# Kernel optimization log

Measured on AMD Instinct MI355X. Metric: run time of the kernel, lower is better.

## Reference

```python
import jax, jax.numpy as jnp
import numpy as np

B, S, D, H, DK, DV, DFF = 2, 2048, 512, 8, 64, 64, 2048
EPS = 1e-5

def layer_norm(x, g, b):
    mu = jnp.mean(x, axis=-1, keepdims=True)
    var = jnp.mean(jnp.square(x - mu), axis=-1, keepdims=True)
    return (x - mu) * jax.lax.rsqrt(var + EPS) * g + b

def setup_inputs() -> dict:
    key = jax.random.key(0)
    ks = jax.random.split(key, 12)
    s = 0.02
    return {
        "enc_inputs": jax.random.normal(ks[0], (B, S, D), dtype=jnp.float32),
        "attn_mask": jax.random.randint(ks[1], (B, S, S), 0, 2) == 1,
        "Wq": jax.random.normal(ks[2], (D, H * DK), dtype=jnp.float32) * s,
        "bq": jnp.zeros((H * DK,), jnp.float32),
        "Wk": jax.random.normal(ks[3], (D, H * DK), dtype=jnp.float32) * s,
        "bk": jnp.zeros((H * DK,), jnp.float32),
        "Wv": jax.random.normal(ks[4], (D, H * DV), dtype=jnp.float32) * s,
        "bv": jnp.zeros((H * DV,), jnp.float32),
        "Wo": jax.random.normal(ks[5], (H * DV, D), dtype=jnp.float32) * s,
        "bo": jnp.zeros((D,), jnp.float32),
        "ln1_g": jnp.ones((D,), jnp.float32),
        "ln1_b": jnp.zeros((D,), jnp.float32),
        "W1": jax.random.normal(ks[6], (D, DFF), dtype=jnp.float32) * s,
        "b1": jnp.zeros((DFF,), jnp.float32),
        "W2": jax.random.normal(ks[7], (DFF, D), dtype=jnp.float32) * s,
        "b2": jnp.zeros((D,), jnp.float32),
        "ln2_g": jnp.ones((D,), jnp.float32),
        "ln2_b": jnp.zeros((D,), jnp.float32),
    }

def reference(enc_inputs, attn_mask, Wq, bq, Wk, bk, Wv, bv, Wo, bo,
              ln1_g, ln1_b, W1, b1, W2, b2, ln2_g, ln2_b):
    x = enc_inputs
    # projections -> [B, H, S, dk/dv]
    q = (x @ Wq + bq).reshape(B, S, H, DK).transpose(0, 2, 1, 3)
    k = (x @ Wk + bk).reshape(B, S, H, DK).transpose(0, 2, 1, 3)
    v = (x @ Wv + bv).reshape(B, S, H, DV).transpose(0, 2, 1, 3)
    scores = jnp.einsum('bhqd,bhkd->bhqk', q, k) / np.sqrt(DK).astype(np.float32)
    scores = jnp.where(attn_mask[:, None, :, :], jnp.float32(-1e9), scores)
    attn = jax.nn.softmax(scores, axis=-1)  # [B,H,S,S]
    context = jnp.einsum('bhqk,bhkd->bhqd', attn, v)
    context = context.transpose(0, 2, 1, 3).reshape(B, S, H * DV)
    attn_out = layer_norm(context @ Wo + bo + x, ln1_g, ln1_b)
    # position-wise FFN (1x1 convs == per-token linears)
    h = jax.nn.relu(attn_out @ W1 + b1)
    ffn_out = h @ W2 + b2
    out = layer_norm(ffn_out + attn_out, ln2_g, ln2_b)
    return out, attn
```

## Files before the change

### kernel.cpp

```cpp
#include <hip/hip_runtime.h>
#include <hip/hip_bf16.h>

typedef __bf16 bf16;
typedef __bf16 bf16x8 __attribute__((ext_vector_type(8)));
typedef __bf16 bf16x4 __attribute__((ext_vector_type(4)));
typedef float f32x4 __attribute__((ext_vector_type(4)));

#define S_LEN 2048
#define D_MOD 512
#define NHEAD 8
#define DHEAD 64
#define NBATCH 2

#define GLOAD_LDS(g, l) __builtin_amdgcn_global_load_lds( \
    (const __attribute__((address_space(1))) unsigned int*)(g), \
    (__attribute__((address_space(3))) unsigned int*)(l), 16, 0, 0)

__global__ void detect_kernel(const unsigned char* __restrict__ m, int* __restrict__ flags) {
    __shared__ int s4[4];
    int t = threadIdx.x;
    if (t < 4) s4[t] = 0;
    __syncthreads();
    int c3F = 0, c80p0 = 0, cnzo = 0;
    for (int i = t; i < 4096; i += 256) {
        unsigned b = m[i];
        c3F += (b == 0x3F);
        c80p0 += ((b == 0x80) && ((i & 3) == 0));
        cnzo += ((b != 0) && ((i & 3) != 0));
    }
    atomicAdd(&s4[1], c3F);
    atomicAdd(&s4[2], c80p0);
    atomicAdd(&s4[3], cnzo);
    __syncthreads();
    if (t == 0) {
        int mode;
        if (s4[1] > 0)      mode = (s4[2] > 0) ? 2 : 0;
        else if (s4[3] > 0) mode = 1;
        else                mode = 0;
        flags[1] = mode;
    }
}

__global__ void maskconv_kernel(const unsigned char* __restrict__ m,
                                const int* __restrict__ flags,
                                unsigned char* __restrict__ out) {
    long i = ((long)blockIdx.x * 256 + threadIdx.x) * 4;
    int mode = flags[1];
    uchar4 v;
    if (mode == 0) {
        const int* mi = (const int*)m;
        v.x = (unsigned char)(mi[i + 0] != 0);
        v.y = (unsigned char)(mi[i + 1] != 0);
        v.z = (unsigned char)(mi[i + 2] != 0);
        v.w = (unsigned char)(mi[i + 3] != 0);
    } else if (mode == 1) {
        uchar4 r = *(const uchar4*)(m + i);
        v.x = (r.x != 0); v.y = (r.y != 0); v.z = (r.z != 0); v.w = (r.w != 0);
    } else {
        const unsigned short* ms = (const unsigned short*)m;
        v.x = (unsigned char)(ms[i + 0] != 0);
        v.y = (unsigned char)(ms[i + 1] != 0);
        v.z = (unsigned char)(ms[i + 2] != 0);
        v.w = (unsigned char)(ms[i + 3] != 0);
    }
    *(uchar4*)(out + i) = v;
}

__global__ __launch_bounds__(256) void packA(const float* __restrict__ src,
                                             bf16* __restrict__ outh,
                                             bf16* __restrict__ outl) {
    long i = ((long)blockIdx.x * 256 + threadIdx.x) * 4;
    f32x4 v = *(const f32x4*)(src + i);
    bf16x4 h, l;
    #pragma unroll
    for (int j = 0; j < 4; ++j) {
        bf16 hh = (bf16)v[j];
        h[j] = hh;
        l[j] = (bf16)(v[j] - (float)hh);
    }
    *(bf16x4*)(outh + i) = h;
    *(bf16x4*)(outl + i) = l;
}

__global__ __launch_bounds__(256) void packWT(const float* __restrict__ W,
                                              bf16* __restrict__ outh,
                                              bf16* __restrict__ outl,
                                              int K, int N) {
    __shared__ float tile[64][65];
    int n0 = blockIdx.x * 64, k0 = blockIdx.y * 64;
    int t = threadIdx.x, tx = t & 63, ty = t >> 6;
    #pragma unroll
    for (int r = ty; r < 64; r += 4)
        tile[r][tx] = W[(long)(k0 + r) * N + n0 + tx];
    __syncthreads();
    #pragma unroll
    for (int r = ty; r < 64; r += 4) {
        float v = tile[tx][r];
        bf16 h = (bf16)v;
        long idx = (long)(n0 + r) * K + k0 + tx;
        outh[idx] = h;
        outl[idx] = (bf16)(v - (float)h);
    }
}

__global__ void concat_bias(const float* __restrict__ a, const float* __restrict__ b,
                            const float* __restrict__ c, float* __restrict__ o) {
    int t = blockIdx.x * 256 + threadIdx.x;
    o[t] = (t < 512) ? a[t] : (t < 1024 ? b[t - 512] : c[t - 1024]);
}

template<int BM, int BN, int WR, int WC, int EPI>
__global__ __launch_bounds__(256) void mgemm(
    const bf16* __restrict__ Ahi, const bf16* __restrict__ Alo,
    const bf16* __restrict__ Bth, const bf16* __restrict__ Btl,
    const float* __restrict__ bias, const float* __restrict__ res,
    float* __restrict__ outf, bf16* __restrict__ outh, bf16* __restrict__ outl,
    int M, int N, int K)
{
    constexpr int WM = BM / WR, WN = BN / WC;
    constexpr int FI = WM / 16, FJ = WN / 16;
    constexpr int NCH = (2 * BM + 2 * BN) / 16;
    constexpr int NPW = NCH / 4;
    __shared__ bf16 lds[(2 * BM + 2 * BN) * 32];

    int t = threadIdx.x;
    int lane = t & 63, wave = t >> 6;
    int lm = lane & 15, quad = lane >> 4;
    int wr = wave / WC, wc = wave % WC;
    int m0 = blockIdx.y * BM, n0 = blockIdx.x * BN;

    const bf16* gp[NPW];
    #pragma unroll
    for (int ci = 0; ci < NPW; ++ci) {
        int c = wave * NPW + ci;
        const bf16* src; int row0;
        if (c < BM / 16)                  { src = Ahi; row0 = m0 + c * 16; }
        else if (c < 2 * BM / 16)         { src = Alo; row0 = m0 + (c - BM / 16) * 16; }
        else if (c < (2 * BM + BN) / 16)  { src = Bth; row0 = n0 + (c - 2 * BM / 16) * 16; }
        else                              { src = Btl; row0 = n0 + (c - (2 * BM + BN) / 16) * 16; }
        gp[ci] = src + (long)(row0 + (lane >> 2)) * K + (lane & 3) * 8;
    }
    bf16* ldsw = &lds[wave * NPW * 512];

    f32x4 acc[FI][FJ] = {};

    for (int k0 = 0; k0 < K; k0 += 32) {
        __syncthreads();
        #pragma unroll
        for (int ci = 0; ci < NPW; ++ci)
            GLOAD_LDS(gp[ci] + k0, ldsw + ci * 512);
        __syncthreads();

        bf16x8 ah[FI], al[FI];
        #pragma unroll
        for (int i = 0; i < FI; ++i) {
            int row = wr * WM + i * 16 + lm;
            ah[i] = *(const bf16x8*)&lds[row * 32 + quad * 8];
            al[i] = *(const bf16x8*)&lds[(BM + row) * 32 + quad * 8];
        }
        #pragma unroll
        for (int j = 0; j < FJ; ++j) {
            int row = wc * WN + j * 16 + lm;
            bf16x8 bh = *(const bf16x8*)&lds[(2 * BM + row) * 32 + quad * 8];
            bf16x8 bl = *(const bf16x8*)&lds[(2 * BM + BN + row) * 32 + quad * 8];
            #pragma unroll
            for (int i = 0; i < FI; ++i) {
                acc[i][j] = __builtin_amdgcn_mfma_f32_16x16x32_bf16(ah[i], bh, acc[i][j], 0, 0, 0);
                acc[i][j] = __builtin_amdgcn_mfma_f32_16x16x32_bf16(ah[i], bl, acc[i][j], 0, 0, 0);
                acc[i][j] = __builtin_amdgcn_mfma_f32_16x16x32_bf16(al[i], bh, acc[i][j], 0, 0, 0);
            }
        }
    }

    #pragma unroll
    for (int j = 0; j < FJ; ++j) {
        int gn = n0 + wc * WN + j * 16 + lm;
        float bv = bias[gn];
        #pragma unroll
        for (int i = 0; i < FI; ++i) {
            #pragma unroll
            for (int r = 0; r < 4; ++r) {
                int gm = m0 + wr * WM + i * 16 + quad * 4 + r;
                float v = acc[i][j][r] + bv;
                if (EPI == 3) {
                    if (gn < 512)       outh[(long)gm * 512 + gn] = (bf16)v;
                    else if (gn < 1024) outl[(long)gm * 512 + gn - 512] = (bf16)v;
                    else                outf[(long)gm * 512 + gn - 1024] = v;
                } else {
                    long idx = (long)gm * N + gn;
                    if (EPI == 1) {
                        v = fmaxf(v, 0.f);
                        bf16 h = (bf16)v;
                        outh[idx] = h;
                        outl[idx] = (bf16)(v - (float)h);
                    } else {
                        if (EPI == 2) v += res[idx];
                        outf[idx] = v;
                    }
                }
            }
        }
    }
}

__global__ __launch_bounds__(256) void pack_vT(const float* __restrict__ src,
                                               bf16* __restrict__ dst) {
    __shared__ float tile[64][65];
    int s0 = blockIdx.x * 64;
    int bh = blockIdx.y;
    int b = bh >> 3, h = bh & 7;
    int t = threadIdx.x, tx = t & 63, ty = t >> 6;
    #pragma unroll
    for (int r = ty; r < 64; r += 4)
        tile[r][tx] = src[(long)(b * S_LEN + s0 + r) * 512 + h * 64 + tx];
    __syncthreads();
    #pragma unroll
    for (int d = ty; d < 64; d += 4)
        dst[((long)bh * 64 + d) * S_LEN + s0 + tx] = (bf16)tile[tx][d];
}

__global__ __launch_bounds__(256) void attn_kernel(
    const bf16* __restrict__ Q, const bf16* __restrict__ Kg,
    const bf16* __restrict__ Vt, const unsigned char* __restrict__ mask8,
    float* __restrict__ attnO, bf16* __restrict__ ctxh, bf16* __restrict__ ctxl)
{
    __shared__ bf16 Qs[64][72];
    __shared__ bf16 Ks[64][72];
    __shared__ bf16 Vs[64][72];
    __shared__ bf16 Ps[64][72];

    int t = threadIdx.x;
    int qt = blockIdx.x & 31, bh = blockIdx.x >> 5;
    int b_ = bh >> 3, h_ = bh & 7;
    int q0 = qt * 64;
    int lane = t & 63, wave = t >> 6;
    int lm = lane & 15, quad = lane >> 4, q8 = quad * 8;
    int sr = t >> 2, sc = (t & 3) * 16;

    const bf16* Qp = Q + (((long)(b_ * S_LEN + q0 + sr)) << 9) + (h_ << 6) + sc;
    *(bf16x8*)&Qs[sr][sc]     = *(const bf16x8*)(Qp);
    *(bf16x8*)&Qs[sr][sc + 8] = *(const bf16x8*)(Qp + 8);
    __syncthreads();
    bf16x8 a0 = *(const bf16x8*)&Qs[wave * 16 + lm][q8];
    bf16x8 a1 = *(const bf16x8*)&Qs[wave * 16 + lm][32 + q8];

    float mrow[4], lrow[4];
    #pragma unroll
    for (int r = 0; r < 4; ++r) { mrow[r] = -1e30f; lrow[r] = 0.f; }

    const unsigned char* Mbase = mask8 + (long)b_ * S_LEN * S_LEN;

    for (int kt = 0; kt < 32; ++kt) {
        int k0 = kt * 64;
        __syncthreads();
        const bf16* Kp = Kg + (((long)(b_ * S_LEN + k0 + sr)) << 9) + (h_ << 6) + sc;
        *(bf16x8*)&Ks[sr][sc]     = *(const bf16x8*)(Kp);
        *(bf16x8*)&Ks[sr][sc + 8] = *(const bf16x8*)(Kp + 8);
        __syncthreads();

        f32x4 sacc[4] = {};
        #pragma unroll
        for (int tn = 0; tn < 4; ++tn) {
            bf16x8 b0 = *(const bf16x8*)&Ks[tn * 16 + lm][q8];
            bf16x8 b1 = *(const bf16x8*)&Ks[tn * 16 + lm][32 + q8];
            sacc[tn] = __builtin_amdgcn_mfma_f32_16x16x32_bf16(a0, b0, sacc[tn], 0, 0, 0);
            sacc[tn] = __builtin_amdgcn_mfma_f32_16x16x32_bf16(a1, b1, sacc[tn], 0, 0, 0);
        }
        #pragma unroll
        for (int r = 0; r < 4; ++r) {
            int grow = q0 + wave * 16 + quad * 4 + r;
            const unsigned char* Mr = Mbase + (long)grow * S_LEN + k0 + lm;
            float sv[4];
            float tmax = -1e30f;
            #pragma unroll
            for (int tn = 0; tn < 4; ++tn) {
                float s = sacc[tn][r] * 0.125f;
                if (Mr[tn * 16]) s = -1e9f;
                sv[tn] = s;
                tmax = fmaxf(tmax, s);
            }
            #pragma unroll
            for (int off = 8; off; off >>= 1) tmax = fmaxf(tmax, __shfl_xor(tmax, off));
            float mnew = fmaxf(mrow[r], tmax);
            float es = 0.f;
            #pragma unroll
            for (int tn = 0; tn < 4; ++tn) es += __expf(sv[tn] - mnew);
            #pragma unroll
            for (int off = 8; off; off >>= 1) es += __shfl_xor(es, off);
            lrow[r] = lrow[r] * __expf(mrow[r] - mnew) + es;
            mrow[r] = mnew;
        }
    }
    float rl[4];
    #pragma unroll
    for (int r = 0; r < 4; ++r) rl[r] = 1.f / lrow[r];

    float* attnBase = attnO + (long)bh * S_LEN * S_LEN;
    const bf16* Vbase = Vt + (long)bh * (DHEAD * S_LEN);
    f32x4 oacc[4] = {};

    for (int kt = 0; kt < 32; ++kt) {
        int k0 = kt * 64;
        __syncthreads();
        const bf16* Kp = Kg + (((long)(b_ * S_LEN + k0 + sr)) << 9) + (h_ << 6) + sc;
        *(bf16x8*)&Ks[sr][sc]     = *(const bf16x8*)(Kp);
        *(bf16x8*)&Ks[sr][sc + 8] = *(const bf16x8*)(Kp + 8);
        const bf16* Vp = Vbase + (long)sr * S_LEN + k0 + sc;
        *(bf16x8*)&Vs[sr][sc]     = *(const bf16x8*)(Vp);
        *(bf16x8*)&Vs[sr][sc + 8] = *(const bf16x8*)(Vp + 8);
        __syncthreads();

        f32x4 sacc[4] = {};
        #pragma unroll
        for (int tn = 0; tn < 4; ++tn) {
            bf16x8 b0 = *(const bf16x8*)&Ks[tn * 16 + lm][q8];
            bf16x8 b1 = *(const bf16x8*)&Ks[tn * 16 + lm][32 + q8];
            sacc[tn] = __builtin_amdgcn_mfma_f32_16x16x32_bf16(a0, b0, sacc[tn], 0, 0, 0);
            sacc[tn] = __builtin_amdgcn_mfma_f32_16x16x32_bf16(a1, b1, sacc[tn], 0, 0, 0);
        }
        #pragma unroll
        for (int r = 0; r < 4; ++r) {
            int grow = q0 + wave * 16 + quad * 4 + r;
            const unsigned char* Mr = Mbase + (long)grow * S_LEN + k0 + lm;
            #pragma unroll
            for (int tn = 0; tn < 4; ++tn) {
                float s = sacc[tn][r] * 0.125f;
                if (Mr[tn * 16]) s = -1e9f;
                float p = __expf(s - mrow[r]) * rl[r];
                attnBase[(long)grow * S_LEN + k0 + tn * 16 + lm] = p;
                Ps[wave * 16 + quad * 4 + r][tn * 16 + lm] = (bf16)p;
            }
        }
        __syncthreads();
        bf16x8 pa0 = *(const bf16x8*)&Ps[wave * 16 + lm][q8];
        bf16x8 pa1 = *(const bf16x8*)&Ps[wave * 16 + lm][32 + q8];
        #pragma unroll
        for (int td = 0; td < 4; ++td) {
            bf16x8 v0 = *(const bf16x8*)&Vs[td * 16 + lm][q8];
            bf16x8 v1 = *(const bf16x8*)&Vs[td * 16 + lm][32 + q8];
            oacc[td] = __builtin_amdgcn_mfma_f32_16x16x32_bf16(pa0, v0, oacc[td], 0, 0, 0);
            oacc[td] = __builtin_amdgcn_mfma_f32_16x16x32_bf16(pa1, v1, oacc[td], 0, 0, 0);
        }
    }

    #pragma unroll
    for (int td = 0; td < 4; ++td)
    #pragma unroll
    for (int r = 0; r < 4; ++r) {
        int grow = q0 + wave * 16 + quad * 4 + r;
        long cidx = (((long)(b_ * S_LEN + grow)) << 9) + (h_ << 6) + td * 16 + lm;
        float v = oacc[td][r];
        bf16 h = (bf16)v;
        ctxh[cidx] = h;
        ctxl[cidx] = (bf16)(v - (float)h);
    }
}

template<int SPLIT>
__global__ __launch_bounds__(256) void ln_kernel(
    const float* __restrict__ X, const float* __restrict__ g,
    const float* __restrict__ bb, float* __restrict__ out,
    bf16* __restrict__ oh, bf16* __restrict__ ol)
{
    __shared__ float red[8];
    int row = blockIdx.x, t = threadIdx.x;
    float x0 = X[(long)row * 512 + t];
    float x1 = X[(long)row * 512 + 256 + t];
    float s = x0 + x1, ss = x0 * x0 + x1 * x1;
    #pragma unroll
    for (int off = 32; off; off >>= 1) { s += __shfl_xor(s, off); ss += __shfl_xor(ss, off); }
    if ((t & 63) == 0) { red[t >> 6] = s; red[4 + (t >> 6)] = ss; }
    __syncthreads();
    float S_ = red[0] + red[1] + red[2] + red[3];
    float SS = red[4] + red[5] + red[6] + red[7];
    float mu = S_ * (1.f / 512.f);
    float var = SS * (1.f / 512.f) - mu * mu;
    float is = rsqrtf(var + 1e-5f);
    float o0 = (x0 - mu) * is * g[t]       + bb[t];
    float o1 = (x1 - mu) * is * g[t + 256] + bb[t + 256];
    out[(long)row * 512 + t]       = o0;
    out[(long)row * 512 + 256 + t] = o1;
    if (SPLIT) {
        bf16 h0 = (bf16)o0, h1 = (bf16)o1;
        oh[(long)row * 512 + t]       = h0;
        oh[(long)row * 512 + 256 + t] = h1;
        ol[(long)row * 512 + t]       = (bf16)(o0 - (float)h0);
        ol[(long)row * 512 + 256 + t] = (bf16)(o1 - (float)h1);
    }
}

extern "C" void kernel_launch(void* const* d_in, const int* in_sizes, int n_in,
                              void* d_out, int out_size, void* d_ws, size_t ws_size,
                              hipStream_t stream)
{
    const float* x = (const float*)d_in[0];
    const unsigned char* maskraw = (const unsigned char*)d_in[1];
    const float* Wq = (const float*)d_in[2];  const float* bq = (const float*)d_in[3];
    const float* Wk = (const float*)d_in[4];  const float* bk = (const float*)d_in[5];
    const float* Wv = (const float*)d_in[6];  const float* bv = (const float*)d_in[7];
    const float* Wo = (const float*)d_in[8];  const float* bo = (const float*)d_in[9];
    const float* ln1g = (const float*)d_in[10]; const float* ln1b = (const float*)d_in[11];
    const float* W1 = (const float*)d_in[12]; const float* b1f = (const float*)d_in[13];
    const float* W2 = (const float*)d_in[14]; const float* b2f = (const float*)d_in[15];
    const float* ln2g = (const float*)d_in[16]; const float* ln2b = (const float*)d_in[17];

    float* outMain = (float*)d_out;
    float* outAttn = outMain + (size_t)NBATCH * S_LEN * D_MOD;

    char* w = (char*)d_ws;
    size_t off = 0;
    auto alloc = [&](size_t bytes) -> char* {
        char* p = w + off;
        off += (bytes + 255) & ~(size_t)255;
        return p;
    };
    const size_t MB = 1024 * 1024;
    int* flags = (int*)alloc(256);
    unsigned char* mask8 = (unsigned char*)alloc(8 * MB);

    bf16* xh   = (bf16*)alloc(4 * MB);
    bf16* xl   = (bf16*)alloc(4 * MB);
    bf16* Qb   = (bf16*)alloc(4 * MB);
    bf16* Kb   = (bf16*)alloc(4 * MB);
    float* vf  = (float*)alloc(8 * MB);
    bf16* Vtb  = (bf16*)alloc(4 * MB);
    bf16* ctxh = (bf16*)alloc(4 * MB);
    bf16* ctxl = (bf16*)alloc(4 * MB);
    bf16* hh = xh;
    bf16* hl = (bf16*)vf;

    float* tmp   = (float*)alloc(8 * MB);
    float* aoutf = (float*)alloc(8 * MB);
    bf16* aouth  = (bf16*)alloc(4 * MB);
    bf16* aoutl  = (bf16*)alloc(4 * MB);

    bf16* WqkvTh = (bf16*)alloc((size_t)1536 * 512 * 2);
    bf16* WqkvTl = (bf16*)alloc((size_t)1536 * 512 * 2);
    bf16* WoTh = (bf16*)alloc(512 * 1024); bf16* WoTl = (bf16*)alloc(512 * 1024);
    bf16* W1Th = (bf16*)alloc(2 * MB);     bf16* W1Tl = (bf16*)alloc(2 * MB);
    bf16* W2Th = (bf16*)alloc(2 * MB);     bf16* W2Tl = (bf16*)alloc(2 * MB);
    float* bqkv = (float*)alloc(1536 * 4);

    const int M = NBATCH * S_LEN;

    detect_kernel<<<1, 256, 0, stream>>>(maskraw, flags);
    maskconv_kernel<<<(NBATCH * S_LEN * S_LEN) / 1024, 256, 0, stream>>>(maskraw, flags, mask8);

    concat_bias<<<6, 256, 0, stream>>>(bq, bk, bv, bqkv);
    packWT<<<dim3(8, 8), 256, 0, stream>>>(Wq, WqkvTh,              WqkvTl,              512, 512);
    packWT<<<dim3(8, 8), 256, 0, stream>>>(Wk, WqkvTh + 512 * 512,  WqkvTl + 512 * 512,  512, 512);
    packWT<<<dim3(8, 8), 256, 0, stream>>>(Wv, WqkvTh + 1024 * 512, WqkvTl + 1024 * 512, 512, 512);
    packWT<<<dim3(8, 8), 256, 0, stream>>>(Wo, WoTh, WoTl, 512, 512);
    packWT<<<dim3(32, 8), 256, 0, stream>>>(W1, W1Th, W1Tl, 512, 2048);
    packWT<<<dim3(8, 32), 256, 0, stream>>>(W2, W2Th, W2Tl, 2048, 512);

    packA<<<(M * 512) / 1024, 256, 0, stream>>>(x, xh, xl);
    mgemm<64, 128, 1, 4, 3><<<dim3(12, 64), 256, 0, stream>>>(
        xh, xl, WqkvTh, WqkvTl, bqkv, nullptr, vf, Qb, Kb, M, 1536, 512);
    pack_vT<<<dim3(32, 16), 256, 0, stream>>>(vf, Vtb);

    attn_kernel<<<512, 256, 0, stream>>>(Qb, Kb, Vtb, mask8, outAttn, ctxh, ctxl);

    mgemm<64, 64, 2, 2, 2><<<dim3(8, 64), 256, 0, stream>>>(
        ctxh, ctxl, WoTh, WoTl, bo, x, tmp, nullptr, nullptr, M, 512, 512);
    ln_kernel<1><<<M, 256, 0, stream>>>(tmp, ln1g, ln1b, aoutf, aouth, aoutl);

    mgemm<128, 128, 2, 2, 1><<<dim3(16, 32), 256, 0, stream>>>(
        aouth, aoutl, W1Th, W1Tl, b1f, nullptr, nullptr, hh, hl, M, 2048, 512);
    mgemm<64, 64, 2, 2, 2><<<dim3(8, 64), 256, 0, stream>>>(
        hh, hl, W2Th, W2Tl, b2f, aoutf, tmp, nullptr, nullptr, M, 512, 2048);
    ln_kernel<0><<<M, 256, 0, stream>>>(tmp, ln2g, ln2b, outMain, nullptr, nullptr);

    (void)in_sizes; (void)n_in; (void)out_size; (void)ws_size;
}
```

Before: 656.5 us.

## Replace two-pass attention with online softmax and in-place attn normalization

The attention kernel drops the separate max/sum pass over K and computes the softmax online in a single loop. Raw masked scores are written to the attn output, the context accumulator is rescaled as the max changes, and at the end each block rereads its attn rows to apply exp and normalization in place. This removes a full QK^T recompute and the second K/mask sweep, at the cost of an extra read-modify-write of the large fp32 attn matrix. It also fuses the three QKV weight-pack launches into one.

```diff
diff --git a/kernel.cpp b/kernel.cpp
--- a/kernel.cpp
+++ b/kernel.cpp
@@ -103,6 +103,30 @@
     }
 }
 
+__global__ __launch_bounds__(256) void packWT3(const float* __restrict__ Wa,
+                                               const float* __restrict__ Wb,
+                                               const float* __restrict__ Wc,
+                                               bf16* __restrict__ outh,
+                                               bf16* __restrict__ outl) {
+    __shared__ float tile[64][65];
+    const float* W = blockIdx.z == 0 ? Wa : (blockIdx.z == 1 ? Wb : Wc);
+    long dofs = (long)blockIdx.z * 512 * 512;
+    int n0 = blockIdx.x * 64, k0 = blockIdx.y * 64;
+    int t = threadIdx.x, tx = t & 63, ty = t >> 6;
+    #pragma unroll
+    for (int r = ty; r < 64; r += 4)
+        tile[r][tx] = W[(long)(k0 + r) * 512 + n0 + tx];
+    __syncthreads();
+    #pragma unroll
+    for (int r = ty; r < 64; r += 4) {
+        float v = tile[tx][r];
+        bf16 h = (bf16)v;
+        long idx = dofs + (long)(n0 + r) * 512 + k0 + tx;
+        outh[idx] = h;
+        outl[idx] = (bf16)(v - (float)h);
+    }
+}
+
 __global__ void concat_bias(const float* __restrict__ a, const float* __restrict__ b,
                             const float* __restrict__ c, float* __restrict__ o) {
     int t = blockIdx.x * 256 + threadIdx.x;
@@ -228,6 +252,8 @@
     __shared__ bf16 Ks[64][72];
     __shared__ bf16 Vs[64][72];
     __shared__ bf16 Ps[64][72];
+    __shared__ float mlds[64];
+    __shared__ float llds[64];
 
     int t = threadIdx.x;
     int qt = blockIdx.x & 31, bh = blockIdx.x >> 5;
@@ -247,57 +273,11 @@
     float mrow[4], lrow[4];
     #pragma unroll
     for (int r = 0; r < 4; ++r) { mrow[r] = -1e30f; lrow[r] = 0.f; }
+    f32x4 oacc[4] = {};
 
     const unsigned char* Mbase = mask8 + (long)b_ * S_LEN * S_LEN;
-
-    for (int kt = 0; kt < 32; ++kt) {
-        int k0 = kt * 64;
-        __syncthreads();
-        const bf16* Kp = Kg + (((long)(b_ * S_LEN + k0 + sr)) << 9) + (h_ << 6) + sc;
-        *(bf16x8*)&Ks[sr][sc]     = *(const bf16x8*)(Kp);
-        *(bf16x8*)&Ks[sr][sc + 8] = *(const bf16x8*)(Kp + 8);
-        __syncthreads();
-
-        f32x4 sacc[4] = {};
-        #pragma unroll
-        for (int tn = 0; tn < 4; ++tn) {
-            bf16x8 b0 = *(const bf16x8*)&Ks[tn * 16 + lm][q8];
-            bf16x8 b1 = *(const bf16x8*)&Ks[tn * 16 + lm][32 + q8];
-            sacc[tn] = __builtin_amdgcn_mfma_f32_16x16x32_bf16(a0, b0, sacc[tn], 0, 0, 0);
-            sacc[tn] = __builtin_amdgcn_mfma_f32_16x16x32_bf16(a1, b1, sacc[tn], 0, 0, 0);
-        }
-        #pragma unroll
-        for (int r = 0; r < 4; ++r) {
-            int grow = q0 + wave * 16 + quad * 4 + r;
-            const unsigned char* Mr = Mbase + (long)grow * S_LEN + k0 + lm;
-            float sv[4];
-            float tmax = -1e30f;
-            #pragma unroll
-            for (int tn = 0; tn < 4; ++tn) {
-                float s = sacc[tn][r] * 0.125f;
-                if (Mr[tn * 16]) s = -1e9f;
-                sv[tn] = s;
-                tmax = fmaxf(tmax, s);
-            }
-            #pragma unroll
-            for (int off = 8; off; off >>= 1) tmax = fmaxf(tmax, __shfl_xor(tmax, off));
-            float mnew = fmaxf(mrow[r], tmax);
-            float es = 0.f;
-            #pragma unroll
-            for (int tn = 0; tn < 4; ++tn) es += __expf(sv[tn] - mnew);
-            #pragma unroll
-            for (int off = 8; off; off >>= 1) es += __shfl_xor(es, off);
-            lrow[r] = lrow[r] * __expf(mrow[r] - mnew) + es;
-            mrow[r] = mnew;
-        }
-    }
-    float rl[4];
-    #pragma unroll
-    for (int r = 0; r < 4; ++r) rl[r] = 1.f / lrow[r];
-
     float* attnBase = attnO + (long)bh * S_LEN * S_LEN;
     const bf16* Vbase = Vt + (long)bh * (DHEAD * S_LEN);
-    f32x4 oacc[4] = {};
 
     for (int kt = 0; kt < 32; ++kt) {
         int k0 = kt * 64;
@@ -318,19 +298,44 @@
             sacc[tn] = __builtin_amdgcn_mfma_f32_16x16x32_bf16(a0, b0, sacc[tn], 0, 0, 0);
             sacc[tn] = __builtin_amdgcn_mfma_f32_16x16x32_bf16(a1, b1, sacc[tn], 0, 0, 0);
         }
+
+        float scr[4];
         #pragma unroll
         for (int r = 0; r < 4; ++r) {
             int grow = q0 + wave * 16 + quad * 4 + r;
             const unsigned char* Mr = Mbase + (long)grow * S_LEN + k0 + lm;
+            float sv[4];
+            float tmax = -1e30f;
             #pragma unroll
             for (int tn = 0; tn < 4; ++tn) {
                 float s = sacc[tn][r] * 0.125f;
                 if (Mr[tn * 16]) s = -1e9f;
-                float p = __expf(s - mrow[r]) * rl[r];
-                attnBase[(long)grow * S_LEN + k0 + tn * 16 + lm] = p;
-                Ps[wave * 16 + quad * 4 + r][tn * 16 + lm] = (bf16)p;
+                sv[tn] = s;
+                tmax = fmaxf(tmax, s);
+                attnBase[(long)grow * S_LEN + k0 + tn * 16 + lm] = s;
             }
-        }
+            #pragma unroll
+            for (int off = 8; off; off >>= 1) tmax = fmaxf(tmax, __shfl_xor(tmax, off));
+            float mnew = fmaxf(mrow[r], tmax);
+            float sc0 = __expf(mrow[r] - mnew);
+            float es = 0.f;
+            #pragma unroll
+            for (int tn = 0; tn < 4; ++tn) {
+                float pe = __expf(sv[tn] - mnew);
+                es += pe;
+                Ps[wave * 16 + quad * 4 + r][tn * 16 + lm] = (bf16)pe;
+            }
+            #pragma unroll
+            for (int off = 8; off; off >>= 1) es += __shfl_xor(es, off);
+            lrow[r] = lrow[r] * sc0 + es;
+            mrow[r] = mnew;
+            scr[r] = sc0;
+        }
+        #pragma unroll
+        for (int td = 0; td < 4; ++td)
+            #pragma unroll
+            for (int r = 0; r < 4; ++r) oacc[td][r] *= scr[r];
+
         __syncthreads();
         bf16x8 pa0 = *(const bf16x8*)&Ps[wave * 16 + lm][q8];
         bf16x8 pa1 = *(const bf16x8*)&Ps[wave * 16 + lm][32 + q8];
@@ -343,16 +348,42 @@
         }
     }
 
+    float rl[4];
+    #pragma unroll
+    for (int r = 0; r < 4; ++r) rl[r] = 1.f / lrow[r];
+
     #pragma unroll
     for (int td = 0; td < 4; ++td)
     #pragma unroll
     for (int r = 0; r < 4; ++r) {
         int grow = q0 + wave * 16 + quad * 4 + r;
         long cidx = (((long)(b_ * S_LEN + grow)) << 9) + (h_ << 6) + td * 16 + lm;
-        float v = oacc[td][r];
+        float v = oacc[td][r] * rl[r];
         bf16 h = (bf16)v;
         ctxh[cidx] = h;
         ctxl[cidx] = (bf16)(v - (float)h);
+    }
+
+    if (lm == 0) {
+        #pragma unroll
+        for (int r = 0; r < 4; ++r) {
+            int row = wave * 16 + quad * 4 + r;
+            mlds[row] = mrow[r];
+            llds[row] = rl[r];
+        }
+    }
+    __syncthreads();
+    int rr = t >> 2;
+    float m_ = mlds[rr], rl_ = llds[rr];
+    f32x4* base = (f32x4*)(attnBase + (((long)(q0 + rr)) << 11) + (t & 3) * 512);
+    #pragma unroll 4
+    for (int i = 0; i < 128; ++i) {
+        f32x4 v = base[i];
+        v[0] = __expf(v[0] - m_) * rl_;
+        v[1] = __expf(v[1] - m_) * rl_;
+        v[2] = __expf(v[2] - m_) * rl_;
+        v[3] = __expf(v[3] - m_) * rl_;
+        base[i] = v;
     }
 }
 
@@ -447,9 +478,7 @@
     maskconv_kernel<<<(NBATCH * S_LEN * S_LEN) / 1024, 256, 0, stream>>>(maskraw, flags, mask8);
 
     concat_bias<<<6, 256, 0, stream>>>(bq, bk, bv, bqkv);
-    packWT<<<dim3(8, 8), 256, 0, stream>>>(Wq, WqkvTh,              WqkvTl,              512, 512);
-    packWT<<<dim3(8, 8), 256, 0, stream>>>(Wk, WqkvTh + 512 * 512,  WqkvTl + 512 * 512,  512, 512);
-    packWT<<<dim3(8, 8), 256, 0, stream>>>(Wv, WqkvTh + 1024 * 512, WqkvTl + 1024 * 512, 512, 512);
+    packWT3<<<dim3(8, 8, 3), 256, 0, stream>>>(Wq, Wk, Wv, WqkvTh, WqkvTl);
     packWT<<<dim3(8, 8), 256, 0, stream>>>(Wo, WoTh, WoTl, 512, 512);
     packWT<<<dim3(32, 8), 256, 0, stream>>>(W1, W1Th, W1Tl, 512, 2048);
     packWT<<<dim3(8, 32), 256, 0, stream>>>(W2, W2Th, W2Tl, 2048, 512);
```

After: 789.1 us. 20.2% more time.

## Double-buffer K/V tiles via async global-to-LDS loads and merge weight packing kernels

Applied to the files above, without the earlier changes.

The attention kernel now prefetches the next K and V tiles straight into swizzled, double-buffered LDS with global_load_lds, so loads overlap the current tile's MFMA and softmax work and two barriers per iteration become one. The XOR swizzle replaces the padded layout to avoid LDS bank conflicts. Six weight-transpose launches and the bias concat are merged into one kernel to cut launch overhead. The cost is more LDS per block, which may lower occupancy, and subtle ordering around the Ps buffer and the async-load completion.

```diff
diff --git a/kernel.cpp b/kernel.cpp
--- a/kernel.cpp
+++ b/kernel.cpp
@@ -82,13 +82,36 @@
     *(bf16x4*)(outl + i) = l;
 }
 
-__global__ __launch_bounds__(256) void packWT(const float* __restrict__ W,
-                                              bf16* __restrict__ outh,
-                                              bf16* __restrict__ outl,
-                                              int K, int N) {
+__global__ __launch_bounds__(256) void packW_all(
+    const float* __restrict__ Wq, const float* __restrict__ Wk,
+    const float* __restrict__ Wv, const float* __restrict__ Wo,
+    const float* __restrict__ W1, const float* __restrict__ W2,
+    const float* __restrict__ bq, const float* __restrict__ bk,
+    const float* __restrict__ bv,
+    bf16* __restrict__ WqkvTh, bf16* __restrict__ WqkvTl,
+    bf16* __restrict__ WoTh, bf16* __restrict__ WoTl,
+    bf16* __restrict__ W1Th, bf16* __restrict__ W1Tl,
+    bf16* __restrict__ W2Th, bf16* __restrict__ W2Tl,
+    float* __restrict__ bqkv)
+{
     __shared__ float tile[64][65];
-    int n0 = blockIdx.x * 64, k0 = blockIdx.y * 64;
-    int t = threadIdx.x, tx = t & 63, ty = t >> 6;
+    int blk = blockIdx.x, t = threadIdx.x;
+    if (blk >= 768) {
+        int i = (blk - 768) * 256 + t;
+        bqkv[i] = (i < 512) ? bq[i] : (i < 1024 ? bk[i - 512] : bv[i - 1024]);
+        return;
+    }
+    const float* W; bf16* oh; bf16* ol; int K, N, lb, sh; long dofs = 0;
+    if (blk < 256) {
+        lb = blk & 63; K = 512; N = 512; sh = 3;
+        if (blk < 64)       { W = Wq; oh = WqkvTh; ol = WqkvTl; }
+        else if (blk < 128) { W = Wk; oh = WqkvTh; ol = WqkvTl; dofs = 512 * 512; }
+        else if (blk < 192) { W = Wv; oh = WqkvTh; ol = WqkvTl; dofs = (long)2 * 512 * 512; }
+        else                { W = Wo; oh = WoTh;   ol = WoTl; }
+    } else if (blk < 512) { lb = blk - 256; W = W1; oh = W1Th; ol = W1Tl; K = 512;  N = 2048; sh = 5; }
+    else                  { lb = blk - 512; W = W2; oh = W2Th; ol = W2Tl; K = 2048; N = 512;  sh = 3; }
+    int n0 = (lb & ((1 << sh) - 1)) * 64, k0 = (lb >> sh) * 64;
+    int tx = t & 63, ty = t >> 6;
     #pragma unroll
     for (int r = ty; r < 64; r += 4)
         tile[r][tx] = W[(long)(k0 + r) * N + n0 + tx];
@@ -97,16 +120,10 @@
     for (int r = ty; r < 64; r += 4) {
         float v = tile[tx][r];
         bf16 h = (bf16)v;
-        long idx = (long)(n0 + r) * K + k0 + tx;
-        outh[idx] = h;
-        outl[idx] = (bf16)(v - (float)h);
-    }
-}
-
-__global__ void concat_bias(const float* __restrict__ a, const float* __restrict__ b,
-                            const float* __restrict__ c, float* __restrict__ o) {
-    int t = blockIdx.x * 256 + threadIdx.x;
-    o[t] = (t < 512) ? a[t] : (t < 1024 ? b[t - 512] : c[t - 1024]);
+        long idx = dofs + (long)(n0 + r) * K + k0 + tx;
+        oh[idx] = h;
+        ol[idx] = (bf16)(v - (float)h);
+    }
 }
 
 template<int BM, int BN, int WR, int WC, int EPI>
@@ -225,8 +242,8 @@
     float* __restrict__ attnO, bf16* __restrict__ ctxh, bf16* __restrict__ ctxl)
 {
     __shared__ bf16 Qs[64][72];
-    __shared__ bf16 Ks[64][72];
-    __shared__ bf16 Vs[64][72];
+    __shared__ bf16 Ks[2][64 * 64];
+    __shared__ bf16 Vs[2][64 * 64];
     __shared__ bf16 Ps[64][72];
 
     int t = threadIdx.x;
@@ -237,6 +254,9 @@
     int lm = lane & 15, quad = lane >> 4, q8 = quad * 8;
     int sr = t >> 2, sc = (t & 3) * 16;
 
+    int srow8 = lane >> 3;
+    int sslot = (lane & 7) ^ srow8;
+
     const bf16* Qp = Q + (((long)(b_ * S_LEN + q0 + sr)) << 9) + (h_ << 6) + sc;
     *(bf16x8*)&Qs[sr][sc]     = *(const bf16x8*)(Qp);
     *(bf16x8*)&Qs[sr][sc + 8] = *(const bf16x8*)(Qp + 8);
@@ -249,97 +269,129 @@
     for (int r = 0; r < 4; ++r) { mrow[r] = -1e30f; lrow[r] = 0.f; }
 
     const unsigned char* Mbase = mask8 + (long)b_ * S_LEN * S_LEN;
-
-    for (int kt = 0; kt < 32; ++kt) {
-        int k0 = kt * 64;
+    const bf16* Kbase = Kg + (((long)(b_ * S_LEN)) << 9) + (h_ << 6);
+    const bf16* Vbase = Vt + (long)bh * (DHEAD * S_LEN);
+
+    {
+        #pragma unroll
+        for (int c = 0; c < 2; ++c) {
+            int rl = wave * 16 + c * 8;
+            GLOAD_LDS(Kbase + (long)(rl + srow8) * 512 + sslot * 8, &Ks[0][rl * 64]);
+        }
         __syncthreads();
-        const bf16* Kp = Kg + (((long)(b_ * S_LEN + k0 + sr)) << 9) + (h_ << 6) + sc;
-        *(bf16x8*)&Ks[sr][sc]     = *(const bf16x8*)(Kp);
-        *(bf16x8*)&Ks[sr][sc + 8] = *(const bf16x8*)(Kp + 8);
+        int cur = 0;
+        for (int kt = 0; kt < 32; ++kt) {
+            int k0 = kt * 64;
+            if (kt < 31) {
+                #pragma unroll
+                for (int c = 0; c < 2; ++c) {
+                    int rl = wave * 16 + c * 8;
+                    GLOAD_LDS(Kbase + (long)(k0 + 64 + rl + srow8) * 512 + sslot * 8,
+                              &Ks[cur ^ 1][rl * 64]);
+                }
+            }
+            const bf16* kc = Ks[cur];
+            f32x4 sacc[4] = {};
+            #pragma unroll
+            for (int tn = 0; tn < 4; ++tn) {
+                int row = tn * 16 + lm, sw = row & 7;
+                bf16x8 b0 = *(const bf16x8*)&kc[row * 64 + ((quad ^ sw) << 3)];
+                bf16x8 b1 = *(const bf16x8*)&kc[row * 64 + (((4 | quad) ^ sw) << 3)];
+                sacc[tn] = __builtin_amdgcn_mfma_f32_16x16x32_bf16(a0, b0, sacc[tn], 0, 0, 0);
+                sacc[tn] = __builtin_amdgcn_mfma_f32_16x16x32_bf16(a1, b1, sacc[tn], 0, 0, 0);
+            }
+            #pragma unroll
+            for (int r = 0; r < 4; ++r) {
+                int grow = q0 + wave * 16 + quad * 4 + r;
+                const unsigned char* Mr = Mbase + (long)grow * S_LEN + k0 + lm;
+                float sv[4];
+                float tmax = -1e30f;
+                #pragma unroll
+                for (int tn = 0; tn < 4; ++tn) {
+                    float s = sacc[tn][r] * 0.125f;
+                    if (Mr[tn * 16]) s = -1e9f;
+                    sv[tn] = s;
+                    tmax = fmaxf(tmax, s);
+                }
+                #pragma unroll
+                for (int off = 8; off; off >>= 1) tmax = fmaxf(tmax, __shfl_xor(tmax, off));
+                float mnew = fmaxf(mrow[r], tmax);
+                float es = 0.f;
+                #pragma unroll
+                for (int tn = 0; tn < 4; ++tn) es += __expf(sv[tn] - mnew);
+                #pragma unroll
+                for (int off = 8; off; off >>= 1) es += __shfl_xor(es, off);
+                lrow[r] = lrow[r] * __expf(mrow[r] - mnew) + es;
+                mrow[r] = mnew;
+            }
+            __syncthreads();
+            cur ^= 1;
+        }
+    }
+    float rl4[4];
+    #pragma unroll
+    for (int r = 0; r < 4; ++r) rl4[r] = 1.f / lrow[r];
+
+    float* attnBase = attnO + (long)bh * S_LEN * S_LEN;
+    f32x4 oacc[4] = {};
+
+    {
+        #pragma unroll
+        for (int c = 0; c < 2; ++c) {
+            int rl = wave * 16 + c * 8;
+            GLOAD_LDS(Kbase + (long)(rl + srow8) * 512 + sslot * 8, &Ks[0][rl * 64]);
+            GLOAD_LDS(Vbase + (long)(rl + srow8) * S_LEN + sslot * 8, &Vs[0][rl * 64]);
+        }
         __syncthreads();
-
-        f32x4 sacc[4] = {};
-        #pragma unroll
-        for (int tn = 0; tn < 4; ++tn) {
-            bf16x8 b0 = *(const bf16x8*)&Ks[tn * 16 + lm][q8];
-            bf16x8 b1 = *(const bf16x8*)&Ks[tn * 16 + lm][32 + q8];
-            sacc[tn] = __builtin_amdgcn_mfma_f32_16x16x32_bf16(a0, b0, sacc[tn], 0, 0, 0);
-            sacc[tn] = __builtin_amdgcn_mfma_f32_16x16x32_bf16(a1, b1, sacc[tn], 0, 0, 0);
-        }
-        #pragma unroll
-        for (int r = 0; r < 4; ++r) {
-            int grow = q0 + wave * 16 + quad * 4 + r;
-            const unsigned char* Mr = Mbase + (long)grow * S_LEN + k0 + lm;
-            float sv[4];
-            float tmax = -1e30f;
+        int cur = 0;
+        for (int kt = 0; kt < 32; ++kt) {
+            int k0 = kt * 64;
+            if (kt < 31) {
+                #pragma unroll
+                for (int c = 0; c < 2; ++c) {
+                    int rl = wave * 16 + c * 8;
+                    GLOAD_LDS(Kbase + (long)(k0 + 64 + rl + srow8) * 512 + sslot * 8,
+                              &Ks[cur ^ 1][rl * 64]);
+                    GLOAD_LDS(Vbase + (long)(rl + srow8) * S_LEN + k0 + 64 + sslot * 8,
+                              &Vs[cur ^ 1][rl * 64]);
+                }
+            }
+            const bf16* kc = Ks[cur];
+            const bf16* vc = Vs[cur];
+            f32x4 sacc[4] = {};
             #pragma unroll
             for (int tn = 0; tn < 4; ++tn) {
-                float s = sacc[tn][r] * 0.125f;
-                if (Mr[tn * 16]) s = -1e9f;
-                sv[tn] = s;
-                tmax = fmaxf(tmax, s);
-            }
-            #pragma unroll
-            for (int off = 8; off; off >>= 1) tmax = fmaxf(tmax, __shfl_xor(tmax, off));
-            float mnew = fmaxf(mrow[r], tmax);
-            float es = 0.f;
-            #pragma unroll
-            for (int tn = 0; tn < 4; ++tn) es += __expf(sv[tn] - mnew);
-            #pragma unroll
-            for (int off = 8; off; off >>= 1) es += __shfl_xor(es, off);
-            lrow[r] = lrow[r] * __expf(mrow[r] - mnew) + es;
-            mrow[r] = mnew;
-        }
-    }
-    float rl[4];
-    #pragma unroll
-    for (int r = 0; r < 4; ++r) rl[r] = 1.f / lrow[r];
-
-    float* attnBase = attnO + (long)bh * S_LEN * S_LEN;
-    const bf16* Vbase = Vt + (long)bh * (DHEAD * S_LEN);
-    f32x4 oacc[4] = {};
-
-    for (int kt = 0; kt < 32; ++kt) {
-        int k0 = kt * 64;
-        __syncthreads();
-        const bf16* Kp = Kg + (((long)(b_ * S_LEN + k0 + sr)) << 9) + (h_ << 6) + sc;
-        *(bf16x8*)&Ks[sr][sc]     = *(const bf16x8*)(Kp);
-        *(bf16x8*)&Ks[sr][sc + 8] = *(const bf16x8*)(Kp + 8);
-        const bf16* Vp = Vbase + (long)sr * S_LEN + k0 + sc;
-        *(bf16x8*)&Vs[sr][sc]     = *(const bf16x8*)(Vp);
-        *(bf16x8*)&Vs[sr][sc + 8] = *(const bf16x8*)(Vp + 8);
-        __syncthreads();
-
-        f32x4 sacc[4] = {};
-        #pragma unroll
-        for (int tn = 0; tn < 4; ++tn) {
-            bf16x8 b0 = *(const bf16x8*)&Ks[tn * 16 + lm][q8];
-            bf16x8 b1 = *(const bf16x8*)&Ks[tn * 16 + lm][32 + q8];
-            sacc[tn] = __builtin_amdgcn_mfma_f32_16x16x32_bf16(a0, b0, sacc[tn], 0, 0, 0);
-            sacc[tn] = __builtin_amdgcn_mfma_f32_16x16x32_bf16(a1, b1, sacc[tn], 0, 0, 0);
-        }
-        #pragma unroll
-        for (int r = 0; r < 4; ++r) {
-            int grow = q0 + wave * 16 + quad * 4 + r;
-            const unsigned char* Mr = Mbase + (long)grow * S_LEN + k0 + lm;
-            #pragma unroll
-            for (int tn = 0; tn < 4; ++tn) {
-                float s = sacc[tn][r] * 0.125f;
-                if (Mr[tn * 16]) s = -1e9f;
-                float p = __expf(s - mrow[r]) * rl[r];
-                attnBase[(long)grow * S_LEN + k0 + tn * 16 + lm] = p;
-                Ps[wave * 16 + quad * 4 + r][tn * 16 + lm] = (bf16)p;
-            }
-        }
-        __syncthreads();
-        bf16x8 pa0 = *(const bf16x8*)&Ps[wave * 16 + lm][q8];
-        bf16x8 pa1 = *(const bf16x8*)&Ps[wave * 16 + lm][32 + q8];
-        #pragma unroll
-        for (int td = 0; td < 4; ++td) {
-            bf16x8 v0 = *(const bf16x8*)&Vs[td * 16 + lm][q8];
-            bf16x8 v1 = *(const bf16x8*)&Vs[td * 16 + lm][32 + q8];
-            oacc[td] = __builtin_amdgcn_mfma_f32_16x16x32_bf16(pa0, v0, oacc[td], 0, 0, 0);
-            oacc[td] = __builtin_amdgcn_mfma_f32_16x16x32_bf16(pa1, v1, oacc[td], 0, 0, 0);
+                int row = tn * 16 + lm, sw = row & 7;
+                bf16x8 b0 = *(const bf16x8*)&kc[row * 64 + ((quad ^ sw) << 3)];
+                bf16x8 b1 = *(const bf16x8*)&kc[row * 64 + (((4 | quad) ^ sw) << 3)];
+                sacc[tn] = __builtin_amdgcn_mfma_f32_16x16x32_bf16(a0, b0, sacc[tn], 0, 0, 0);
+                sacc[tn] = __builtin_amdgcn_mfma_f32_16x16x32_bf16(a1, b1, sacc[tn], 0, 0, 0);
+            }
+            #pragma unroll
+            for (int r = 0; r < 4; ++r) {
+                int grow = q0 + wave * 16 + quad * 4 + r;
+                const unsigned char* Mr = Mbase + (long)grow * S_LEN + k0 + lm;
+                #pragma unroll
+                for (int tn = 0; tn < 4; ++tn) {
+                    float s = sacc[tn][r] * 0.125f;
+                    if (Mr[tn * 16]) s = -1e9f;
+                    float p = __expf(s - mrow[r]) * rl4[r];
+                    attnBase[(long)grow * S_LEN + k0 + tn * 16 + lm] = p;
+                    Ps[wave * 16 + quad * 4 + r][tn * 16 + lm] = (bf16)p;
+                }
+            }
+            bf16x8 pa0 = *(const bf16x8*)&Ps[wave * 16 + lm][q8];
+            bf16x8 pa1 = *(const bf16x8*)&Ps[wave * 16 + lm][32 + q8];
+            #pragma unroll
+            for (int td = 0; td < 4; ++td) {
+                int row = td * 16 + lm, sw = row & 7;
+                bf16x8 v0 = *(const bf16x8*)&vc[row * 64 + ((quad ^ sw) << 3)];
+                bf16x8 v1 = *(const bf16x8*)&vc[row * 64 + (((4 | quad) ^ sw) << 3)];
+                oacc[td] = __builtin_amdgcn_mfma_f32_16x16x32_bf16(pa0, v0, oacc[td], 0, 0, 0);
+                oacc[td] = __builtin_amdgcn_mfma_f32_16x16x32_bf16(pa1, v1, oacc[td], 0, 0, 0);
+            }
+            __syncthreads();
+            cur ^= 1;
         }
     }
 
@@ -446,13 +498,9 @@
     detect_kernel<<<1, 256, 0, stream>>>(maskraw, flags);
     maskconv_kernel<<<(NBATCH * S_LEN * S_LEN) / 1024, 256, 0, stream>>>(maskraw, flags, mask8);
 
-    concat_bias<<<6, 256, 0, stream>>>(bq, bk, bv, bqkv);
-    packWT<<<dim3(8, 8), 256, 0, stream>>>(Wq, WqkvTh,              WqkvTl,              512, 512);
-    packWT<<<dim3(8, 8), 256, 0, stream>>>(Wk, WqkvTh + 512 * 512,  WqkvTl + 512 * 512,  512, 512);
-    packWT<<<dim3(8, 8), 256, 0, stream>>>(Wv, WqkvTh + 1024 * 512, WqkvTl + 1024 * 512, 512, 512);
-    packWT<<<dim3(8, 8), 256, 0, stream>>>(Wo, WoTh, WoTl, 512, 512);
-    packWT<<<dim3(32, 8), 256, 0, stream>>>(W1, W1Th, W1Tl, 512, 2048);
-    packWT<<<dim3(8, 32), 256, 0, stream>>>(W2, W2Th, W2Tl, 2048, 512);
+    packW_all<<<774, 256, 0, stream>>>(Wq, Wk, Wv, Wo, W1, W2, bq, bk, bv,
+                                       WqkvTh, WqkvTl, WoTh, WoTl,
+                                       W1Th, W1Tl, W2Th, W2Tl, bqkv);
 
     packA<<<(M * 512) / 1024, 256, 0, stream>>>(x, xh, xl);
     mgemm<64, 128, 1, 4, 3><<<dim3(12, 64), 256, 0, stream>>>(
```

Measured after the change: 614.0 us. -6.5%, faster.
